# Kernel optimization log

Measured on AMD Instinct MI355X. Metric: run time of the kernel, lower is better.

## Reference

```python
import jax, jax.numpy as jnp
import numpy as np

B, T, F = 64, 1000, 512
H, KD = 8, 32
EPS = 1e-6


def setup_inputs() -> dict:
    key = jax.random.key(0)
    ks = jax.random.split(key, 12)
    s_in = 1.0 / np.sqrt(F)
    s_out = 1.0 / np.sqrt(H * KD)
    return {
        "x": jax.random.normal(ks[0], (B, T, F), jnp.float32),
        "q": jax.random.normal(ks[1], (F,), jnp.float32) * s_in,      # global_query (1,1,F) squeezed
        "Wq": jax.random.normal(ks[2], (F, H, KD), jnp.float32) * s_in,
        "bq": jnp.zeros((H, KD), jnp.float32),
        "Wk": jax.random.normal(ks[3], (F, H, KD), jnp.float32) * s_in,
        "bk": jnp.zeros((H, KD), jnp.float32),
        "Wv": jax.random.normal(ks[4], (F, H, KD), jnp.float32) * s_in,
        "bv": jnp.zeros((H, KD), jnp.float32),
        "Wo": jax.random.normal(ks[5], (H, KD, F), jnp.float32) * s_out,
        "bo": jnp.zeros((F,), jnp.float32),
        "Wd": jax.random.normal(ks[6], (F, F), jnp.float32) * s_in,    # Dense, use_bias=False
        "gamma": jnp.ones((F,), jnp.float32),
        "beta": jnp.zeros((F,), jnp.float32),
    }


def reference(x, q, Wq, bq, Wk, bk, Wv, bv, Wo, bo, Wd, gamma, beta):
    # Single learned query attends over full sequence (keras MultiHeadAttention semantics).
    qh = jnp.einsum('f,fhk->hk', q, Wq) + bq                   # (H, KD), shared across batch
    kh = jnp.einsum('btf,fhk->bthk', x, Wk) + bk               # (B, T, H, KD)
    vh = jnp.einsum('btf,fhk->bthk', x, Wv) + bv               # (B, T, H, KD)
    scale = 1.0 / jnp.sqrt(jnp.asarray(KD, x.dtype))
    scores = jnp.einsum('hk,bthk->bht', qh, kh) * scale        # (B, H, T)
    attn = jax.nn.softmax(scores, axis=-1)
    ctx = jnp.einsum('bht,bthk->bhk', attn, vh)                # (B, H, KD)
    pooled = jnp.einsum('bhk,hkf->bf', ctx, Wo) + bo           # (B, F) attention output proj
    out = pooled @ Wd                                          # Dense, no bias
    mu = jnp.mean(out, axis=-1, keepdims=True)
    var = jnp.mean(jnp.square(out - mu), axis=-1, keepdims=True)
    return (out - mu) * jax.lax.rsqrt(var + EPS) * gamma + beta
```

## Files before the change

kernel.cpp:

```cpp
#include <hip/hip_runtime.h>
#include <cstddef>

#define B_ 64
#define T_ 1000
#define F_ 512
#define H_ 8
#define KD_ 32
#define HK_ 256
#define NC_ 16

__global__ __launch_bounds__(64) void k_qh(const float* __restrict__ q,
                                           const float* __restrict__ Wq,
                                           const float* __restrict__ bq,
                                           float* __restrict__ qh) {
    int hk = blockIdx.x;
    int lane = threadIdx.x;
    float s = 0.f;
    for (int f = lane; f < F_; f += 64) s += q[f] * Wq[(size_t)f * HK_ + hk];
    #pragma unroll
    for (int off = 32; off; off >>= 1) s += __shfl_down(s, off);
    if (lane == 0) qh[hk] = s + bq[hk];
}

__global__ __launch_bounds__(256) void k_wk(const float* __restrict__ qh,
                                            const float* __restrict__ Wk,
                                            const float* __restrict__ bk,
                                            float* __restrict__ wk,
                                            float* __restrict__ ck) {
    int f = blockIdx.x;
    int tid = threadIdx.x;
    __shared__ float red[256];
    red[tid] = qh[tid] * Wk[(size_t)f * HK_ + tid];
    __syncthreads();
    #pragma unroll
    for (int off = 16; off; off >>= 1) {
        if ((tid & 31) < off) red[tid] += red[tid + off];
        __syncthreads();
    }
    if ((tid & 31) == 0) wk[f * H_ + (tid >> 5)] = red[tid];
    if (f == 0 && tid < H_) {
        float c = 0.f;
        for (int k = 0; k < KD_; k++) c += qh[tid * KD_ + k] * bk[tid * KD_ + k];
        ck[tid] = c;
    }
}

__global__ __launch_bounds__(256) void k_fused(const float* __restrict__ x,
                                               const float* __restrict__ wk,
                                               const float* __restrict__ ck,
                                               float* __restrict__ part,
                                               float* __restrict__ ml) {
    int c = blockIdx.x & (NC_ - 1);
    int b = blockIdx.x >> 4;
    int nt = (c < 8) ? 63 : 62;
    int t0 = (c < 8) ? c * 63 : 504 + (c - 8) * 62;
    int tid = threadIdx.x;
    int lane = tid & 63, w = tid >> 6;

    __shared__ float sp[H_][65];

    {
        int f0 = lane * 8;
        float wreg[8][8];
        #pragma unroll
        for (int i = 0; i < 8; i++)
            #pragma unroll
            for (int h = 0; h < H_; h++) wreg[i][h] = wk[(f0 + i) * H_ + h];
        float ckv = ck[lane >> 3];
        const float scale = 0.17677669529663687f;

        for (int tl = w; tl < nt; tl += 4) {
            const float4* xr = (const float4*)(x + ((size_t)(b * T_ + t0 + tl)) * F_ + f0);
            float4 a = xr[0], bb = xr[1];
            float xv[8] = {a.x, a.y, a.z, a.w, bb.x, bb.y, bb.z, bb.w};
            float acc[8];
            #pragma unroll
            for (int h = 0; h < H_; h++) acc[h] = 0.f;
            #pragma unroll
            for (int i = 0; i < 8; i++)
                #pragma unroll
                for (int h = 0; h < H_; h++) acc[h] += xv[i] * wreg[i][h];
            #pragma unroll
            for (int h = 0; h < H_; h++) {
                acc[h] += __shfl_xor(acc[h], 8);
                acc[h] += __shfl_xor(acc[h], 16);
                acc[h] += __shfl_xor(acc[h], 32);
            }
            float v = acc[0];
            #pragma unroll
            for (int h = 1; h < H_; h++) v = ((lane >> 3) == h) ? acc[h] : v;
            v += __shfl_xor(v, 1);
            v += __shfl_xor(v, 2);
            v += __shfl_xor(v, 4);
            if ((lane & 7) == 0) sp[lane >> 3][tl] = (v + ckv) * scale;
        }
    }
    __syncthreads();

    {
        int g = tid >> 5, j = tid & 31;
        float m = -1e30f;
        #pragma unroll
        for (int i = 0; i < 2; i++) { int t = j + 32 * i; if (t < nt) m = fmaxf(m, sp[g][t]); }
        #pragma unroll
        for (int off = 16; off; off >>= 1) m = fmaxf(m, __shfl_xor(m, off));
        float l = 0.f;
        float e0 = 0.f, e1 = 0.f;
        { int t = j;      if (t < nt) { e0 = __expf(sp[g][t] - m); l += e0; } }
        { int t = j + 32; if (t < nt) { e1 = __expf(sp[g][t] - m); l += e1; } }
        __syncthreads();
        { int t = j;      if (t < nt) sp[g][t] = e0; }
        { int t = j + 32; if (t < nt) sp[g][t] = e1; }
        #pragma unroll
        for (int off = 16; off; off >>= 1) l += __shfl_xor(l, off);
        if (j == 0) {
            float* d = ml + ((size_t)(c * B_ + b) * H_ + g) * 2;
            d[0] = m; d[1] = l;
        }
    }
    __syncthreads();

    {
        float acc[H_][2];
        #pragma unroll
        for (int h = 0; h < H_; h++) { acc[h][0] = 0.f; acc[h][1] = 0.f; }
        const float2* xb = (const float2*)(x + ((size_t)(b * T_ + t0)) * F_) + tid;
        for (int tt = 0; tt < nt; tt++) {
            float2 xv = xb[(size_t)tt * 256];
            #pragma unroll
            for (int h = 0; h < H_; h++) {
                float a = sp[h][tt];
                acc[h][0] += a * xv.x;
                acc[h][1] += a * xv.y;
            }
        }
        float2* dst = (float2*)(part + (size_t)(c * B_ + b) * (H_ * F_));
        #pragma unroll
        for (int h = 0; h < H_; h++)
            dst[h * (F_ / 2) + tid] = make_float2(acc[h][0], acc[h][1]);
    }
}

__global__ __launch_bounds__(512) void k_tail(const float* __restrict__ part,
                                              const float* __restrict__ ml,
                                              const float* __restrict__ Wv,
                                              const float* __restrict__ bv,
                                              const float* __restrict__ Wo,
                                              const float* __restrict__ bo,
                                              const float* __restrict__ Wd,
                                              const float* __restrict__ gamma,
                                              const float* __restrict__ beta,
                                              float* __restrict__ out) {
    int b = blockIdx.x;
    int tid = threadIdx.x;
    __shared__ float coefs[NC_][H_];
    __shared__ float xs[H_ * F_];
    __shared__ float ctx_s[HK_];
    __shared__ float pooled_s[F_];
    __shared__ float red[512];
    __shared__ float stat[2];

    if (tid < H_) {
        int h = tid;
        float M = -1e30f;
        #pragma unroll
        for (int c = 0; c < NC_; c++)
            M = fmaxf(M, ml[((size_t)(c * B_ + b) * H_ + h) * 2]);
        float L = 0.f;
        #pragma unroll
        for (int c = 0; c < NC_; c++) {
            const float* d = ml + ((size_t)(c * B_ + b) * H_ + h) * 2;
            L += __expf(d[0] - M) * d[1];
        }
        float invL = 1.0f / L;
        #pragma unroll
        for (int c = 0; c < NC_; c++) {
            const float* d = ml + ((size_t)(c * B_ + b) * H_ + h) * 2;
            coefs[c][h] = __expf(d[0] - M) * invL;
        }
    }
    __syncthreads();

    for (int i = tid; i < H_ * F_; i += 512) {
        int h = i >> 9;
        float s = 0.f;
        #pragma unroll
        for (int c = 0; c < NC_; c++)
            s += coefs[c][h] * part[(size_t)(c * B_ + b) * (H_ * F_) + i];
        xs[i] = s;
    }
    __syncthreads();

    {
        int hk = tid & 255;
        int half = tid >> 8;
        int h = hk >> 5;
        float s = 0.f;
        int fb = half * 256;
        for (int j = 0; j < 256; j++) {
            int f = fb + j;
            s += xs[h * F_ + f] * Wv[(size_t)f * HK_ + hk];
        }
        red[tid] = s;
        __syncthreads();
        if (tid < 256) ctx_s[tid] = red[tid] + red[tid + 256] + bv[tid];
    }
    __syncthreads();

    {
        float s = 0.f;
        for (int hk = 0; hk < HK_; hk++) s += ctx_s[hk] * Wo[(size_t)hk * F_ + tid];
        pooled_s[tid] = s + bo[tid];
    }
    __syncthreads();

    float o = 0.f;
    for (int g = 0; g < F_; g++) o += pooled_s[g] * Wd[(size_t)g * F_ + tid];

    {
        float v1 = o, v2 = o * o;
        #pragma unroll
        for (int off = 32; off; off >>= 1) {
            v1 += __shfl_down(v1, off);
            v2 += __shfl_down(v2, off);
        }
        int lane = tid & 63, wid = tid >> 6;
        if (lane == 0) { red[wid] = v1; red[8 + wid] = v2; }
        __syncthreads();
        if (tid == 0) {
            float s1 = 0.f, s2 = 0.f;
            #pragma unroll
            for (int w = 0; w < 8; w++) { s1 += red[w]; s2 += red[8 + w]; }
            float mu = s1 * (1.0f / F_);
            float var = s2 * (1.0f / F_) - mu * mu;
            stat[0] = mu;
            stat[1] = rsqrtf(var + 1e-6f);
        }
        __syncthreads();
    }
    float mu = stat[0], rstd = stat[1];
    out[(size_t)b * F_ + tid] = (o - mu) * rstd * gamma[tid] + beta[tid];
}

extern "C" void kernel_launch(void* const* d_in, const int* in_sizes, int n_in,
                              void* d_out, int out_size, void* d_ws, size_t ws_size,
                              hipStream_t stream) {
    const float* x     = (const float*)d_in[0];
    const float* q     = (const float*)d_in[1];
    const float* Wq    = (const float*)d_in[2];
    const float* bq    = (const float*)d_in[3];
    const float* Wk    = (const float*)d_in[4];
    const float* bk    = (const float*)d_in[5];
    const float* Wv    = (const float*)d_in[6];
    const float* bv    = (const float*)d_in[7];
    const float* Wo    = (const float*)d_in[8];
    const float* bo    = (const float*)d_in[9];
    const float* Wd    = (const float*)d_in[10];
    const float* gamma = (const float*)d_in[11];
    const float* beta  = (const float*)d_in[12];
    float* out = (float*)d_out;

    char* ws = (char*)d_ws;
    float* qh   = (float*)(ws + 0);
    float* wk   = (float*)(ws + 4096);
    float* ck   = (float*)(ws + 20480);
    float* ml   = (float*)(ws + 24576);
    float* part = (float*)(ws + 1048576);

    k_qh<<<HK_, 64, 0, stream>>>(q, Wq, bq, qh);
    k_wk<<<F_, 256, 0, stream>>>(qh, Wk, bk, wk, ck);
    k_fused<<<B_ * NC_, 256, 0, stream>>>(x, wk, ck, part, ml);
    k_tail<<<B_, 512, 0, stream>>>(part, ml, Wv, bv, Wo, bo, Wd, gamma, beta, out);
}
```

Measured before the change: 291.3 us.

## Fold Wo·Wd into one weight, split V projection into parallel kernel, double chunks

Precomputes Weff = Wo·Wd and bo·Wd once per call, so the tail does a single 256x512 matvec instead of two chained projections. It also moves the per-chunk Wv projection into a separate, more parallel k_ctx kernel that projects each chunk's weighted-x partials before they are combined. T is split into 32 chunks instead of 16, which doubles the number of fused blocks. The cost is an extra 256x512x512 weight GEMM per call done with naive per-thread loops, two extra launches, and more partial traffic.

```diff
diff --git a/kernel.cpp b/kernel.cpp
--- a/kernel.cpp
+++ b/kernel.cpp
@@ -7,7 +7,7 @@
 #define H_ 8
 #define KD_ 32
 #define HK_ 256
-#define NC_ 16
+#define NC_ 32
 
 __global__ __launch_bounds__(64) void k_qh(const float* __restrict__ q,
                                            const float* __restrict__ Wq,
@@ -45,19 +45,38 @@
     }
 }
 
+__global__ __launch_bounds__(512) void k_weff(const float* __restrict__ Wo,
+                                              const float* __restrict__ Wd,
+                                              const float* __restrict__ bo,
+                                              float* __restrict__ weff,
+                                              float* __restrict__ bwd) {
+    int blk = blockIdx.x;
+    int f = threadIdx.x;
+    if (blk < HK_) {
+        const float* wo = Wo + (size_t)blk * F_;
+        float s = 0.f;
+        for (int g = 0; g < F_; g++) s += wo[g] * Wd[(size_t)g * F_ + f];
+        weff[(size_t)blk * F_ + f] = s;
+    } else {
+        float s = 0.f;
+        for (int g = 0; g < F_; g++) s += bo[g] * Wd[(size_t)g * F_ + f];
+        bwd[f] = s;
+    }
+}
+
 __global__ __launch_bounds__(256) void k_fused(const float* __restrict__ x,
                                                const float* __restrict__ wk,
                                                const float* __restrict__ ck,
                                                float* __restrict__ part,
                                                float* __restrict__ ml) {
     int c = blockIdx.x & (NC_ - 1);
-    int b = blockIdx.x >> 4;
-    int nt = (c < 8) ? 63 : 62;
-    int t0 = (c < 8) ? c * 63 : 504 + (c - 8) * 62;
+    int b = blockIdx.x >> 5;
+    int nt = (c < 8) ? 32 : 31;
+    int t0 = (c < 8) ? c * 32 : 256 + (c - 8) * 31;
     int tid = threadIdx.x;
     int lane = tid & 63, w = tid >> 6;
 
-    __shared__ float sp[H_][65];
+    __shared__ float sp[H_][33];
 
     {
         int f0 = lane * 8;
@@ -100,17 +119,14 @@
     {
         int g = tid >> 5, j = tid & 31;
         float m = -1e30f;
-        #pragma unroll
-        for (int i = 0; i < 2; i++) { int t = j + 32 * i; if (t < nt) m = fmaxf(m, sp[g][t]); }
+        if (j < nt) m = sp[g][j];
         #pragma unroll
         for (int off = 16; off; off >>= 1) m = fmaxf(m, __shfl_xor(m, off));
-        float l = 0.f;
-        float e0 = 0.f, e1 = 0.f;
-        { int t = j;      if (t < nt) { e0 = __expf(sp[g][t] - m); l += e0; } }
-        { int t = j + 32; if (t < nt) { e1 = __expf(sp[g][t] - m); l += e1; } }
-        __syncthreads();
-        { int t = j;      if (t < nt) sp[g][t] = e0; }
-        { int t = j + 32; if (t < nt) sp[g][t] = e1; }
+        float e0 = 0.f;
+        if (j < nt) e0 = __expf(sp[g][j] - m);
+        float l = e0;
+        __syncthreads();
+        if (j < nt) sp[g][j] = e0;
         #pragma unroll
         for (int off = 16; off; off >>= 1) l += __shfl_xor(l, off);
         if (j == 0) {
@@ -141,23 +157,44 @@
     }
 }
 
-__global__ __launch_bounds__(512) void k_tail(const float* __restrict__ part,
+__global__ __launch_bounds__(256) void k_ctx(const float* __restrict__ part,
+                                             const float* __restrict__ Wv,
+                                             float* __restrict__ pctx) {
+    int b = blockIdx.x & (B_ - 1);
+    int p = blockIdx.x >> 6;
+    int hk = threadIdx.x;
+    int h = hk >> 5;
+    const float* p0 = part + ((size_t)((4 * p + 0) * B_ + b) * H_ + h) * F_;
+    const float* p1 = part + ((size_t)((4 * p + 1) * B_ + b) * H_ + h) * F_;
+    const float* p2 = part + ((size_t)((4 * p + 2) * B_ + b) * H_ + h) * F_;
+    const float* p3 = part + ((size_t)((4 * p + 3) * B_ + b) * H_ + h) * F_;
+    float a0 = 0.f, a1 = 0.f, a2 = 0.f, a3 = 0.f;
+    for (int f = 0; f < F_; f++) {
+        float wv = Wv[(size_t)f * HK_ + hk];
+        a0 += p0[f] * wv;
+        a1 += p1[f] * wv;
+        a2 += p2[f] * wv;
+        a3 += p3[f] * wv;
+    }
+    pctx[((size_t)(4 * p + 0) * B_ + b) * HK_ + hk] = a0;
+    pctx[((size_t)(4 * p + 1) * B_ + b) * HK_ + hk] = a1;
+    pctx[((size_t)(4 * p + 2) * B_ + b) * HK_ + hk] = a2;
+    pctx[((size_t)(4 * p + 3) * B_ + b) * HK_ + hk] = a3;
+}
+
+__global__ __launch_bounds__(512) void k_tail(const float* __restrict__ pctx,
                                               const float* __restrict__ ml,
-                                              const float* __restrict__ Wv,
                                               const float* __restrict__ bv,
-                                              const float* __restrict__ Wo,
-                                              const float* __restrict__ bo,
-                                              const float* __restrict__ Wd,
+                                              const float* __restrict__ weff,
+                                              const float* __restrict__ bwd,
                                               const float* __restrict__ gamma,
                                               const float* __restrict__ beta,
                                               float* __restrict__ out) {
     int b = blockIdx.x;
     int tid = threadIdx.x;
     __shared__ float coefs[NC_][H_];
-    __shared__ float xs[H_ * F_];
     __shared__ float ctx_s[HK_];
-    __shared__ float pooled_s[F_];
-    __shared__ float red[512];
+    __shared__ float red[16];
     __shared__ float stat[2];
 
     if (tid < H_) {
@@ -181,41 +218,18 @@
     }
     __syncthreads();
 
-    for (int i = tid; i < H_ * F_; i += 512) {
-        int h = i >> 9;
+    if (tid < HK_) {
+        int h = tid >> 5;
         float s = 0.f;
         #pragma unroll
         for (int c = 0; c < NC_; c++)
-            s += coefs[c][h] * part[(size_t)(c * B_ + b) * (H_ * F_) + i];
-        xs[i] = s;
-    }
-    __syncthreads();
-
-    {
-        int hk = tid & 255;
-        int half = tid >> 8;
-        int h = hk >> 5;
-        float s = 0.f;
-        int fb = half * 256;
-        for (int j = 0; j < 256; j++) {
-            int f = fb + j;
-            s += xs[h * F_ + f] * Wv[(size_t)f * HK_ + hk];
-        }
-        red[tid] = s;
-        __syncthreads();
-        if (tid < 256) ctx_s[tid] = red[tid] + red[tid + 256] + bv[tid];
-    }
-    __syncthreads();
-
-    {
-        float s = 0.f;
-        for (int hk = 0; hk < HK_; hk++) s += ctx_s[hk] * Wo[(size_t)hk * F_ + tid];
-        pooled_s[tid] = s + bo[tid];
-    }
-    __syncthreads();
-
-    float o = 0.f;
-    for (int g = 0; g < F_; g++) o += pooled_s[g] * Wd[(size_t)g * F_ + tid];
+            s += coefs[c][h] * pctx[((size_t)c * B_ + b) * HK_ + tid];
+        ctx_s[tid] = s + bv[tid];
+    }
+    __syncthreads();
+
+    float o = bwd[tid];
+    for (int hk = 0; hk < HK_; hk++) o += ctx_s[hk] * weff[(size_t)hk * F_ + tid];
 
     {
         float v1 = o, v2 = o * o;
@@ -265,10 +279,15 @@
     float* wk   = (float*)(ws + 4096);
     float* ck   = (float*)(ws + 20480);
     float* ml   = (float*)(ws + 24576);
-    float* part = (float*)(ws + 1048576);
+    float* weff = (float*)(ws + 262144);
+    float* bwd  = (float*)(ws + 786432);
+    float* pctx = (float*)(ws + 1048576);
+    float* part = (float*)(ws + 4194304);
 
     k_qh<<<HK_, 64, 0, stream>>>(q, Wq, bq, qh);
     k_wk<<<F_, 256, 0, stream>>>(qh, Wk, bk, wk, ck);
+    k_weff<<<HK_ + 1, 512, 0, stream>>>(Wo, Wd, bo, weff, bwd);
     k_fused<<<B_ * NC_, 256, 0, stream>>>(x, wk, ck, part, ml);
-    k_tail<<<B_, 512, 0, stream>>>(part, ml, Wv, bv, Wo, bo, Wd, gamma, beta, out);
-}
+    k_ctx<<<(NC_ / 4) * B_, 256, 0, stream>>>(part, Wv, pctx);
+    k_tail<<<B_, 512, 0, stream>>>(pctx, ml, bv, weff, bwd, gamma, beta, out);
+}
```

Result: slower. 317.8 us (+9.1%).

## Fold Wo·Wd into a precomputed weight and restructure the attention chunk kernel

Applied to the files above, without the earlier changes.

A new kernel precomputes weff = Wo·Wd and the bias term bo·Wd using atomic partial sums over a zeroed workspace. The tail kernel then does a single 256-long dot per output instead of two chained projections, which removes the per-batch 512x512 Wd pass. The fused attention kernel now uses 8 chunks of 125 timesteps with 128 threads. Each thread computes a full row's scores with float4 loads, and the weighted-sum pass uses float4 accumulators. This cuts the number of blocks, so there is less parallelism and less coalesced per-thread row reads, and it adds a memset and an extra launch.

```diff
diff --git a/kernel.cpp b/kernel.cpp
--- a/kernel.cpp
+++ b/kernel.cpp
@@ -7,7 +7,8 @@
 #define H_ 8
 #define KD_ 32
 #define HK_ 256
-#define NC_ 16
+#define NC_ 8
+#define CT_ 125
 
 __global__ __launch_bounds__(64) void k_qh(const float* __restrict__ q,
                                            const float* __restrict__ Wq,
@@ -45,138 +46,134 @@
     }
 }
 
-__global__ __launch_bounds__(256) void k_fused(const float* __restrict__ x,
+__global__ __launch_bounds__(512) void k_weff(const float* __restrict__ Wo,
+                                              const float* __restrict__ Wd,
+                                              const float* __restrict__ bo,
+                                              float* __restrict__ weff,
+                                              float* __restrict__ bwd) {
+    int sub = blockIdx.x % 257;
+    int gi = blockIdx.x / 257;
+    int f = threadIdx.x;
+    int g0 = gi * 128;
+    if (sub < HK_) {
+        const float* wo = Wo + (size_t)sub * F_ + g0;
+        float s = 0.f;
+        #pragma unroll 8
+        for (int g = 0; g < 128; g++) s += wo[g] * Wd[(size_t)(g0 + g) * F_ + f];
+        atomicAdd(&weff[(size_t)sub * F_ + f], s);
+    } else {
+        float s = 0.f;
+        #pragma unroll 8
+        for (int g = 0; g < 128; g++) s += bo[g0 + g] * Wd[(size_t)(g0 + g) * F_ + f];
+        atomicAdd(&bwd[f], s);
+    }
+}
+
+__global__ __launch_bounds__(128) void k_fused(const float* __restrict__ x,
                                                const float* __restrict__ wk,
                                                const float* __restrict__ ck,
                                                float* __restrict__ part,
-                                               float* __restrict__ ml) {
-    int c = blockIdx.x & (NC_ - 1);
-    int b = blockIdx.x >> 4;
-    int nt = (c < 8) ? 63 : 62;
-    int t0 = (c < 8) ? c * 63 : 504 + (c - 8) * 62;
-    int tid = threadIdx.x;
-    int lane = tid & 63, w = tid >> 6;
-
-    __shared__ float sp[H_][65];
-
-    {
-        int f0 = lane * 8;
-        float wreg[8][8];
-        #pragma unroll
-        for (int i = 0; i < 8; i++)
-            #pragma unroll
-            for (int h = 0; h < H_; h++) wreg[i][h] = wk[(f0 + i) * H_ + h];
-        float ckv = ck[lane >> 3];
-        const float scale = 0.17677669529663687f;
-
-        for (int tl = w; tl < nt; tl += 4) {
-            const float4* xr = (const float4*)(x + ((size_t)(b * T_ + t0 + tl)) * F_ + f0);
-            float4 a = xr[0], bb = xr[1];
-            float xv[8] = {a.x, a.y, a.z, a.w, bb.x, bb.y, bb.z, bb.w};
-            float acc[8];
-            #pragma unroll
-            for (int h = 0; h < H_; h++) acc[h] = 0.f;
-            #pragma unroll
-            for (int i = 0; i < 8; i++)
+                                               float2* __restrict__ ml2) {
+    __shared__ __align__(16) float at[CT_ + 3][H_];
+    const int c = blockIdx.x & (NC_ - 1);
+    const int b = blockIdx.x >> 3;
+    const int tid = threadIdx.x;
+    const float scale = 0.17677669529663687f;
+
+    if (tid < CT_) {
+        const float4* xr = (const float4*)(x + ((size_t)b * T_ + (size_t)c * CT_ + tid) * F_);
+        float acc[H_] = {0.f,0.f,0.f,0.f,0.f,0.f,0.f,0.f};
+        for (int ii = 0; ii < 16; ii++) {
+            float4 xv[8];
+            #pragma unroll
+            for (int u = 0; u < 8; u++) xv[u] = xr[ii * 8 + u];
+            #pragma unroll
+            for (int u = 0; u < 8; u++) {
+                const float* wr = wk + (size_t)(ii * 8 + u) * 32;
                 #pragma unroll
-                for (int h = 0; h < H_; h++) acc[h] += xv[i] * wreg[i][h];
+                for (int h = 0; h < H_; h++)
+                    acc[h] += xv[u].x * wr[h]      + xv[u].y * wr[8 + h]
+                            + xv[u].z * wr[16 + h] + xv[u].w * wr[24 + h];
+            }
+        }
+        #pragma unroll
+        for (int h = 0; h < H_; h++) at[tid][h] = (acc[h] + ck[h]) * scale;
+    }
+    __syncthreads();
+
+    {
+        const int h = tid >> 4, j = tid & 15;
+        float m = -3.0e38f;
+        for (int t = j; t < CT_; t += 16) m = fmaxf(m, at[t][h]);
+        #pragma unroll
+        for (int off = 8; off; off >>= 1) m = fmaxf(m, __shfl_xor(m, off, 16));
+        float l = 0.f;
+        for (int t = j; t < CT_; t += 16) {
+            float p = __expf(at[t][h] - m);
+            at[t][h] = p;
+            l += p;
+        }
+        #pragma unroll
+        for (int off = 8; off; off >>= 1) l += __shfl_xor(l, off, 16);
+        if (j == 0) ml2[(size_t)(c * B_ + b) * H_ + h] = make_float2(m, l);
+    }
+    __syncthreads();
+
+    {
+        const float4* xc = (const float4*)(x + ((size_t)b * T_ + (size_t)c * CT_) * F_) + tid;
+        float4 a[H_];
+        #pragma unroll
+        for (int h = 0; h < H_; h++) a[h] = make_float4(0.f, 0.f, 0.f, 0.f);
+        #pragma unroll 5
+        for (int t = 0; t < CT_; t++) {
+            const float4 xv = xc[(size_t)t * 128];
             #pragma unroll
             for (int h = 0; h < H_; h++) {
-                acc[h] += __shfl_xor(acc[h], 8);
-                acc[h] += __shfl_xor(acc[h], 16);
-                acc[h] += __shfl_xor(acc[h], 32);
+                const float p = at[t][h];
+                a[h].x += p * xv.x; a[h].y += p * xv.y;
+                a[h].z += p * xv.z; a[h].w += p * xv.w;
             }
-            float v = acc[0];
-            #pragma unroll
-            for (int h = 1; h < H_; h++) v = ((lane >> 3) == h) ? acc[h] : v;
-            v += __shfl_xor(v, 1);
-            v += __shfl_xor(v, 2);
-            v += __shfl_xor(v, 4);
-            if ((lane & 7) == 0) sp[lane >> 3][tl] = (v + ckv) * scale;
-        }
-    }
-    __syncthreads();
-
-    {
-        int g = tid >> 5, j = tid & 31;
-        float m = -1e30f;
-        #pragma unroll
-        for (int i = 0; i < 2; i++) { int t = j + 32 * i; if (t < nt) m = fmaxf(m, sp[g][t]); }
-        #pragma unroll
-        for (int off = 16; off; off >>= 1) m = fmaxf(m, __shfl_xor(m, off));
-        float l = 0.f;
-        float e0 = 0.f, e1 = 0.f;
-        { int t = j;      if (t < nt) { e0 = __expf(sp[g][t] - m); l += e0; } }
-        { int t = j + 32; if (t < nt) { e1 = __expf(sp[g][t] - m); l += e1; } }
-        __syncthreads();
-        { int t = j;      if (t < nt) sp[g][t] = e0; }
-        { int t = j + 32; if (t < nt) sp[g][t] = e1; }
-        #pragma unroll
-        for (int off = 16; off; off >>= 1) l += __shfl_xor(l, off);
-        if (j == 0) {
-            float* d = ml + ((size_t)(c * B_ + b) * H_ + g) * 2;
-            d[0] = m; d[1] = l;
-        }
-    }
-    __syncthreads();
-
-    {
-        float acc[H_][2];
-        #pragma unroll
-        for (int h = 0; h < H_; h++) { acc[h][0] = 0.f; acc[h][1] = 0.f; }
-        const float2* xb = (const float2*)(x + ((size_t)(b * T_ + t0)) * F_) + tid;
-        for (int tt = 0; tt < nt; tt++) {
-            float2 xv = xb[(size_t)tt * 256];
-            #pragma unroll
-            for (int h = 0; h < H_; h++) {
-                float a = sp[h][tt];
-                acc[h][0] += a * xv.x;
-                acc[h][1] += a * xv.y;
-            }
-        }
-        float2* dst = (float2*)(part + (size_t)(c * B_ + b) * (H_ * F_));
-        #pragma unroll
-        for (int h = 0; h < H_; h++)
-            dst[h * (F_ / 2) + tid] = make_float2(acc[h][0], acc[h][1]);
+        }
+        float4* dst = (float4*)(part + (size_t)(c * B_ + b) * (H_ * F_));
+        #pragma unroll
+        for (int h = 0; h < H_; h++) dst[h * 128 + tid] = a[h];
     }
 }
 
 __global__ __launch_bounds__(512) void k_tail(const float* __restrict__ part,
-                                              const float* __restrict__ ml,
+                                              const float2* __restrict__ ml2,
                                               const float* __restrict__ Wv,
                                               const float* __restrict__ bv,
-                                              const float* __restrict__ Wo,
-                                              const float* __restrict__ bo,
-                                              const float* __restrict__ Wd,
+                                              const float* __restrict__ weff,
+                                              const float* __restrict__ bwd,
                                               const float* __restrict__ gamma,
                                               const float* __restrict__ beta,
                                               float* __restrict__ out) {
     int b = blockIdx.x;
     int tid = threadIdx.x;
-    __shared__ float coefs[NC_][H_];
+    __shared__ float coef[NC_][H_];
     __shared__ float xs[H_ * F_];
     __shared__ float ctx_s[HK_];
-    __shared__ float pooled_s[F_];
     __shared__ float red[512];
     __shared__ float stat[2];
 
     if (tid < H_) {
         int h = tid;
-        float M = -1e30f;
+        float M = -3.0e38f;
         #pragma unroll
         for (int c = 0; c < NC_; c++)
-            M = fmaxf(M, ml[((size_t)(c * B_ + b) * H_ + h) * 2]);
+            M = fmaxf(M, ml2[(size_t)(c * B_ + b) * H_ + h].x);
         float L = 0.f;
         #pragma unroll
         for (int c = 0; c < NC_; c++) {
-            const float* d = ml + ((size_t)(c * B_ + b) * H_ + h) * 2;
-            L += __expf(d[0] - M) * d[1];
+            float2 d = ml2[(size_t)(c * B_ + b) * H_ + h];
+            L += __expf(d.x - M) * d.y;
         }
         float invL = 1.0f / L;
         #pragma unroll
         for (int c = 0; c < NC_; c++) {
-            const float* d = ml + ((size_t)(c * B_ + b) * H_ + h) * 2;
-            coefs[c][h] = __expf(d[0] - M) * invL;
+            float2 d = ml2[(size_t)(c * B_ + b) * H_ + h];
+            coef[c][h] = __expf(d.x - M) * invL;
         }
     }
     __syncthreads();
@@ -186,7 +183,7 @@
         float s = 0.f;
         #pragma unroll
         for (int c = 0; c < NC_; c++)
-            s += coefs[c][h] * part[(size_t)(c * B_ + b) * (H_ * F_) + i];
+            s += coef[c][h] * part[(size_t)(c * B_ + b) * (H_ * F_) + i];
         xs[i] = s;
     }
     __syncthreads();
@@ -195,8 +192,9 @@
         int hk = tid & 255;
         int half = tid >> 8;
         int h = hk >> 5;
-        float s = 0.f;
         int fb = half * 256;
+        float s = 0.f;
+        #pragma unroll 8
         for (int j = 0; j < 256; j++) {
             int f = fb + j;
             s += xs[h * F_ + f] * Wv[(size_t)f * HK_ + hk];
@@ -207,15 +205,9 @@
     }
     __syncthreads();
 
-    {
-        float s = 0.f;
-        for (int hk = 0; hk < HK_; hk++) s += ctx_s[hk] * Wo[(size_t)hk * F_ + tid];
-        pooled_s[tid] = s + bo[tid];
-    }
-    __syncthreads();
-
-    float o = 0.f;
-    for (int g = 0; g < F_; g++) o += pooled_s[g] * Wd[(size_t)g * F_ + tid];
+    float o = bwd[tid];
+    #pragma unroll 8
+    for (int hk = 0; hk < HK_; hk++) o += ctx_s[hk] * weff[(size_t)hk * F_ + tid];
 
     {
         float v1 = o, v2 = o * o;
@@ -230,7 +222,7 @@
         if (tid == 0) {
             float s1 = 0.f, s2 = 0.f;
             #pragma unroll
-            for (int w = 0; w < 8; w++) { s1 += red[w]; s2 += red[8 + w]; }
+            for (int ww = 0; ww < 8; ww++) { s1 += red[ww]; s2 += red[8 + ww]; }
             float mu = s1 * (1.0f / F_);
             float var = s2 * (1.0f / F_) - mu * mu;
             stat[0] = mu;
@@ -261,14 +253,18 @@
     float* out = (float*)d_out;
 
     char* ws = (char*)d_ws;
-    float* qh   = (float*)(ws + 0);
-    float* wk   = (float*)(ws + 4096);
-    float* ck   = (float*)(ws + 20480);
-    float* ml   = (float*)(ws + 24576);
-    float* part = (float*)(ws + 1048576);
-
+    float*  qh   = (float*)(ws + 0);
+    float*  wk   = (float*)(ws + 4096);
+    float*  ck   = (float*)(ws + 20480);
+    float*  weff = (float*)(ws + 24576);
+    float*  bwd  = (float*)(ws + 548864);
+    float2* ml2  = (float2*)(ws + 557056);
+    float*  part = (float*)(ws + 589824);
+
+    hipMemsetAsync(ws + 24576, 0, 526336, stream);
     k_qh<<<HK_, 64, 0, stream>>>(q, Wq, bq, qh);
     k_wk<<<F_, 256, 0, stream>>>(qh, Wk, bk, wk, ck);
-    k_fused<<<B_ * NC_, 256, 0, stream>>>(x, wk, ck, part, ml);
-    k_tail<<<B_, 512, 0, stream>>>(part, ml, Wv, bv, Wo, bo, Wd, gamma, beta, out);
-}
+    k_weff<<<4 * 257, 512, 0, stream>>>(Wo, Wd, bo, weff, bwd);
+    k_fused<<<B_ * NC_, 128, 0, stream>>>(x, wk, ck, part, ml2);
+    k_tail<<<B_, 512, 0, stream>>>(part, ml2, Wv, bv, weff, bwd, gamma, beta, out);
+}
```

Result: no change. 295.2 us (+1.3%).
